# Kernel tuning notes

Hardware: AMD Instinct MI355X
Metric: run time of the kernel (lower is better)

The kernel has to match this reference:

```python
import jax, jax.numpy as jnp
import numpy as np

N_NODES = 100000

def gcn_conv(x, W, b, src, dst, n_nodes):
    # PyG GCNConv: out[dst] += norm * (x @ W)[src] + b, with self-loops and
    # symmetric normalization norm = deg^-1/2[src] * deg^-1/2[dst].
    loop = jnp.arange(n_nodes, dtype=src.dtype)
    s = jnp.concatenate([src, loop])
    d = jnp.concatenate([dst, loop])
    deg = jax.ops.segment_sum(jnp.ones_like(d, dtype=x.dtype), d, num_segments=n_nodes)
    dinv = jnp.where(deg > 0, jax.lax.rsqrt(deg), 0.0)
    norm = dinv[s] * dinv[d]                      # [E+N]
    h = x @ W                                     # [N, H]
    msg = h[s] * norm[:, None]                    # [E+N, H] gather
    out = jax.ops.segment_sum(msg, d, num_segments=n_nodes)  # scatter-add
    return out + b

def setup_inputs() -> dict:
    key = jax.random.key(0)
    ks = jax.random.split(key, 8)
    in_dim, hidden = 128, 128
    x = jax.random.normal(ks[0], (N_NODES, in_dim), dtype=jnp.float32)
    edge_index = jax.random.randint(ks[1], (2, 1600000), 0, N_NODES, dtype=jnp.int32)
    sc = 1.0 / np.sqrt(in_dim)
    W1 = jax.random.uniform(ks[2], (in_dim, hidden), jnp.float32, -sc, sc)
    b1 = jnp.zeros((hidden,), jnp.float32)
    W2 = jax.random.uniform(ks[3], (hidden, hidden), jnp.float32, -sc, sc)
    b2 = jnp.zeros((hidden,), jnp.float32)
    Wf = jax.random.uniform(ks[4], (hidden, 1), jnp.float32, -sc, sc)
    bf = jnp.zeros((1,), jnp.float32)
    return {"x": x, "W1": W1, "b1": b1, "W2": W2, "b2": b2, "Wf": Wf, "bf": bf, "edge_index": edge_index}

def reference(x, W1, b1, W2, b2, Wf, bf, edge_index):
    src, dst = edge_index[0], edge_index[1]
    h = jax.nn.relu(gcn_conv(x, W1, b1, src, dst, N_NODES))
    h = jax.nn.relu(gcn_conv(h, W2, b2, src, dst, N_NODES))
    out = (h @ Wf + bf).squeeze(-1)               # [N]
    return out
```

## Files before the change

### kernel.cpp

```cpp
#include <hip/hip_runtime.h>


#define FEAT 128
#define BSH 9
#define BNODES 512

typedef __attribute__((ext_vector_type(8))) short  bf16x8;
typedef __attribute__((ext_vector_type(4))) float  f32x4;

static inline size_t align_up(size_t x, size_t a){ return (x + a - 1) & ~(a - 1); }

__device__ __forceinline__ unsigned short f2bf(float f){
  unsigned int u = __float_as_uint(f);
  return (unsigned short)((u + 0x7fffu + ((u >> 16) & 1u)) >> 16);
}
__device__ __forceinline__ float bflo(unsigned int p){ return __uint_as_float(p << 16); }
__device__ __forceinline__ float bfhi(unsigned int p){ return __uint_as_float(p & 0xffff0000u); }


__global__ __launch_bounds__(256) void bin_count_kernel(
    const int* __restrict__ dst, int* __restrict__ bucket_cnt, int E, int chunk)
{
  __shared__ int hist[256];
  int t = threadIdx.x;
  hist[t] = 0;
  __syncthreads();
  int s0 = blockIdx.x * chunk, s1 = min(E, s0 + chunk);
  for (int i = s0 + t; i < s1; i += 256) atomicAdd(&hist[dst[i] >> BSH], 1);
  __syncthreads();
  if (hist[t] > 0) atomicAdd(&bucket_cnt[t], hist[t]);
}

__global__ __launch_bounds__(256) void bucket_scan_kernel(
    int* __restrict__ bucket_cnt, int* __restrict__ bucket_off,
    int* __restrict__ bucket_cur, int* __restrict__ rowptr, int nbk, int N)
{
  __shared__ int sh[256];
  int t = threadIdx.x;
  int v = (t < nbk) ? bucket_cnt[t] : 0;
  sh[t] = v;
  __syncthreads();
  #pragma unroll
  for (int off = 1; off < 256; off <<= 1){
    int add = (t >= off) ? sh[t - off] : 0;
    __syncthreads();
    sh[t] += add;
    __syncthreads();
  }
  if (t < nbk){
    int e = sh[t] - v;
    bucket_off[t] = e;
    bucket_cur[t] = e;
  }
  if (t == 0){
    bucket_off[nbk] = sh[255];
    rowptr[N] = sh[255];
  }
}

__global__ __launch_bounds__(256) void bin_scatter_kernel(
    const int* __restrict__ src, const int* __restrict__ dst,
    int* __restrict__ bucket_cur, unsigned int* __restrict__ packed, int E, int chunk)
{
  __shared__ int hist[256];
  __shared__ int base[256];
  int t = threadIdx.x;
  hist[t] = 0;
  __syncthreads();
  int s0 = blockIdx.x * chunk, s1 = min(E, s0 + chunk);
  for (int i = s0 + t; i < s1; i += 256) atomicAdd(&hist[dst[i] >> BSH], 1);
  __syncthreads();
  int h = hist[t];
  if (h > 0) base[t] = atomicAdd(&bucket_cur[t], h);
  __syncthreads();
  hist[t] = 0;
  __syncthreads();
  for (int i = s0 + t; i < s1; i += 256){
    int d = dst[i];
    int b = d >> BSH;
    int pos = base[b] + atomicAdd(&hist[b], 1);
    packed[pos] = ((unsigned int)src[i] << BSH) | (unsigned int)(d & (BNODES - 1));
  }
}

__global__ __launch_bounds__(512) void bucket_build_kernel(
    const unsigned int* __restrict__ packed, const int* __restrict__ bucket_off,
    float* __restrict__ dinv, int* __restrict__ rowptr, int* __restrict__ colidx, int N)
{
  __shared__ int degl[BNODES];
  __shared__ int scan[BNODES];
  __shared__ int cur[BNODES];
  int b = blockIdx.x;
  int t = threadIdx.x;
  int node0 = b << BSH;
  int e0 = bucket_off[b], e1 = bucket_off[b + 1];

  degl[t] = 0;
  __syncthreads();
  for (int i = e0 + t; i < e1; i += BNODES) atomicAdd(&degl[packed[i] & (BNODES - 1)], 1);
  __syncthreads();

  int d = degl[t];
  int node = node0 + t;
  if (node < N) dinv[node] = rsqrtf((float)(d + 1));

  scan[t] = d;
  __syncthreads();
  #pragma unroll
  for (int off = 1; off < BNODES; off <<= 1){
    int add = (t >= off) ? scan[t - off] : 0;
    __syncthreads();
    scan[t] += add;
    __syncthreads();
  }
  int excl = scan[t] - d;
  if (node < N) rowptr[node] = e0 + excl;
  cur[t] = excl;
  __syncthreads();

  for (int i = e0 + t; i < e1; i += BNODES){
    unsigned int p = packed[i];
    int pos = atomicAdd(&cur[p & (BNODES - 1)], 1);
    colidx[e0 + pos] = (int)(p >> BSH);
  }
}


__global__ __launch_bounds__(256) void wt_convert_kernel(
    const float* __restrict__ W, unsigned short* __restrict__ Wt)
{
  int gid = blockIdx.x * 256 + threadIdx.x;
  int n = gid >> 7, k = gid & 127;
  Wt[gid] = f2bf(W[(size_t)k * FEAT + n]);
}


template<bool INBF>
__global__ __launch_bounds__(256) void gemm_mfma_kernel(
    const void* __restrict__ Ain, const unsigned short* __restrict__ Wt,
    const float* __restrict__ dinv, unsigned short* __restrict__ Cout, int N)
{
  __shared__ unsigned short aT[128 * 128];
  __shared__ unsigned short wT[128 * 128];
  const int t = threadIdx.x;
  const int row0 = blockIdx.x * 128;

  {
    const uint4* s4 = (const uint4*)Wt;
    #pragma unroll
    for (int i = 0; i < 8; ++i){
      int c = t + i * 256;
      int n = c >> 4, k8 = (c & 15) * 8;
      uint4 v = s4[c];
      *reinterpret_cast<uint4*>(&wT[(n * 128 + k8) ^ ((n & 7) << 3)]) = v;
    }
  }
  if (INBF){
    const unsigned short* Ab = (const unsigned short*)Ain;
    #pragma unroll
    for (int i = 0; i < 8; ++i){
      int c = t + i * 256;
      int r = c >> 4, k8 = (c & 15) * 8;
      int row = row0 + r;
      uint4 v = make_uint4(0, 0, 0, 0);
      float s = 0.f;
      if (row < N){ v = *(const uint4*)(Ab + (size_t)row * FEAT + k8); s = dinv[row]; }
      unsigned int wi[4] = {v.x, v.y, v.z, v.w}, o[4];
      #pragma unroll
      for (int j = 0; j < 4; ++j){
        float lo = bflo(wi[j]) * s, hi = bfhi(wi[j]) * s;
        o[j] = (unsigned int)f2bf(lo) | ((unsigned int)f2bf(hi) << 16);
      }
      *reinterpret_cast<uint4*>(&aT[(r * 128 + k8) ^ ((r & 7) << 3)]) = make_uint4(o[0], o[1], o[2], o[3]);
    }
  } else {
    const float* Af = (const float*)Ain;
    #pragma unroll
    for (int i = 0; i < 16; ++i){
      int c = t + i * 256;
      int r = c >> 5, k4 = (c & 31) * 4;
      int row = row0 + r;
      float4 v = make_float4(0, 0, 0, 0);
      float s = 0.f;
      if (row < N){ v = *(const float4*)(Af + (size_t)row * FEAT + k4); s = dinv[row]; }
      ushort4 o;
      o.x = f2bf(v.x * s); o.y = f2bf(v.y * s); o.z = f2bf(v.z * s); o.w = f2bf(v.w * s);
      *reinterpret_cast<ushort4*>(&aT[(r * 128 + k4) ^ ((r & 7) << 3)]) = o;
    }
  }
  __syncthreads();

  const int w = t >> 6, l = t & 63;
  const int wbase = w * 32;
  const int lm = l & 15;
  const int lk = (l >> 4) * 8;

  f32x4 acc[8][2];
  #pragma unroll
  for (int mt = 0; mt < 8; ++mt)
    #pragma unroll
    for (int nt = 0; nt < 2; ++nt) acc[mt][nt] = (f32x4){0.f, 0.f, 0.f, 0.f};

  #pragma unroll
  for (int ks = 0; ks < 4; ++ks){
    int kb = ks * 32 + lk;
    bf16x8 bfr[2], afr[8];
    #pragma unroll
    for (int nt = 0; nt < 2; ++nt){
      int n = wbase + nt * 16 + lm;
      bfr[nt] = *reinterpret_cast<const bf16x8*>(&wT[(n * 128 + kb) ^ ((n & 7) << 3)]);
    }
    #pragma unroll
    for (int mt = 0; mt < 8; ++mt){
      int m = mt * 16 + lm;
      afr[mt] = *reinterpret_cast<const bf16x8*>(&aT[(m * 128 + kb) ^ ((m & 7) << 3)]);
    }
    #pragma unroll
    for (int mt = 0; mt < 8; ++mt)
      #pragma unroll
      for (int nt = 0; nt < 2; ++nt)
        acc[mt][nt] = __builtin_amdgcn_mfma_f32_16x16x32_bf16(afr[mt], bfr[nt], acc[mt][nt], 0, 0, 0);
  }
  __syncthreads();

  #pragma unroll
  for (int mt = 0; mt < 8; ++mt)
    #pragma unroll
    for (int nt = 0; nt < 2; ++nt)
      #pragma unroll
      for (int r = 0; r < 4; ++r){
        int mrow = mt * 16 + (l >> 4) * 4 + r;
        int col  = wbase + nt * 16 + lm;
        aT[mrow * 128 + col] = f2bf(acc[mt][nt][r]);
      }
  __syncthreads();
  #pragma unroll
  for (int i = 0; i < 8; ++i){
    int c = t + i * 256;
    int r = c >> 4, k8 = (c & 15) * 8;
    int row = row0 + r;
    if (row < N)
      *reinterpret_cast<uint4*>(&Cout[(size_t)row * FEAT + k8]) =
          *reinterpret_cast<const uint4*>(&aT[r * 128 + k8]);
  }
}


__global__ __launch_bounds__(256) void aggregate_kernel(
    const unsigned short* __restrict__ Hs, const int* __restrict__ rowptr,
    const int* __restrict__ col, const float* __restrict__ dinv,
    const float* __restrict__ bias, unsigned short* __restrict__ out, int N)
{
  int gid  = blockIdx.x * blockDim.x + threadIdx.x;
  int v    = gid >> 6;
  int lane = threadIdx.x & 63;
  if (v >= N) return;
  const float dv = dinv[v];
  const unsigned int* Hu = (const unsigned int*)Hs;
  int e = rowptr[v], end = rowptr[v + 1];

  unsigned int m = Hu[(size_t)v * 64 + lane];
  float ax = bflo(m), ay = bfhi(m);
  for (; e + 4 <= end; e += 4){
    int u0 = col[e], u1 = col[e + 1], u2 = col[e + 2], u3 = col[e + 3];
    unsigned int p0 = Hu[(size_t)u0 * 64 + lane];
    unsigned int p1 = Hu[(size_t)u1 * 64 + lane];
    unsigned int p2 = Hu[(size_t)u2 * 64 + lane];
    unsigned int p3 = Hu[(size_t)u3 * 64 + lane];
    ax += bflo(p0) + bflo(p1) + bflo(p2) + bflo(p3);
    ay += bfhi(p0) + bfhi(p1) + bfhi(p2) + bfhi(p3);
  }
  for (; e < end; ++e){
    unsigned int p = Hu[(size_t)col[e] * 64 + lane];
    ax += bflo(p); ay += bfhi(p);
  }
  float2 b = *reinterpret_cast<const float2*>(bias + lane * 2);
  float ox = fmaxf(dv * ax + b.x, 0.f);
  float oy = fmaxf(dv * ay + b.y, 0.f);
  ((unsigned int*)out)[(size_t)v * 64 + lane] =
      (unsigned int)f2bf(ox) | ((unsigned int)f2bf(oy) << 16);
}

__global__ __launch_bounds__(256) void aggregate_final_kernel(
    const unsigned short* __restrict__ Hs, const int* __restrict__ rowptr,
    const int* __restrict__ col, const float* __restrict__ dinv,
    const float* __restrict__ bias, const float* __restrict__ Wf,
    const float* __restrict__ bf, float* __restrict__ out, int N)
{
  int gid  = blockIdx.x * blockDim.x + threadIdx.x;
  int v    = gid >> 6;
  int lane = threadIdx.x & 63;
  if (v >= N) return;
  const float dv = dinv[v];
  const unsigned int* Hu = (const unsigned int*)Hs;
  int e = rowptr[v], end = rowptr[v + 1];

  unsigned int m = Hu[(size_t)v * 64 + lane];
  float ax = bflo(m), ay = bfhi(m);
  for (; e + 4 <= end; e += 4){
    int u0 = col[e], u1 = col[e + 1], u2 = col[e + 2], u3 = col[e + 3];
    unsigned int p0 = Hu[(size_t)u0 * 64 + lane];
    unsigned int p1 = Hu[(size_t)u1 * 64 + lane];
    unsigned int p2 = Hu[(size_t)u2 * 64 + lane];
    unsigned int p3 = Hu[(size_t)u3 * 64 + lane];
    ax += bflo(p0) + bflo(p1) + bflo(p2) + bflo(p3);
    ay += bfhi(p0) + bfhi(p1) + bfhi(p2) + bfhi(p3);
  }
  for (; e < end; ++e){
    unsigned int p = Hu[(size_t)col[e] * 64 + lane];
    ax += bflo(p); ay += bfhi(p);
  }
  float2 b = *reinterpret_cast<const float2*>(bias + lane * 2);
  float ox = fmaxf(dv * ax + b.x, 0.f);
  float oy = fmaxf(dv * ay + b.y, 0.f);
  float2 wf = *reinterpret_cast<const float2*>(Wf + lane * 2);
  float p = ox * wf.x + oy * wf.y;
  #pragma unroll
  for (int off = 32; off > 0; off >>= 1) p += __shfl_down(p, off, 64);
  if (lane == 0) out[v] = p + bf[0];
}


extern "C" void kernel_launch(void* const* d_in, const int* in_sizes, int n_in,
                              void* d_out, int out_size, void* d_ws, size_t ws_size,
                              hipStream_t stream)
{
  const float* x   = (const float*)d_in[0];
  const float* W1  = (const float*)d_in[1];
  const float* b1  = (const float*)d_in[2];
  const float* W2  = (const float*)d_in[3];
  const float* b2  = (const float*)d_in[4];
  const float* Wf  = (const float*)d_in[5];
  const float* bfb = (const float*)d_in[6];
  const int*  eidx = (const int*)d_in[7];

  const int N = in_sizes[0] / FEAT;
  const int E = in_sizes[7] / 2;
  const int* src = eidx;
  const int* dst = eidx + E;
  const int NBK = (N + BNODES - 1) >> BSH;

  char* ws = (char*)d_ws;
  size_t off = 0;
  auto alloc = [&](size_t bytes){ void* p = ws + off; off = align_up(off + bytes, 256); return p; };
  unsigned short* A    = (unsigned short*)alloc((size_t)N * FEAT * 2);
  unsigned short* B    = (unsigned short*)alloc((size_t)N * FEAT * 2);
  unsigned short* Wt1  = (unsigned short*)alloc((size_t)FEAT * FEAT * 2);
  unsigned short* Wt2  = (unsigned short*)alloc((size_t)FEAT * FEAT * 2);
  float* dinv   = (float*)alloc((size_t)N * 4);
  int*   rowptr = (int*)  alloc((size_t)(N + 1) * 4);
  int*   colidx = (int*)  alloc((size_t)E * 4);
  unsigned int* packed = (unsigned int*)alloc((size_t)E * 4);
  int*   bcnt   = (int*)  alloc(256 * 4);
  int*   boff   = (int*)  alloc(257 * 4);
  int*   bcur   = (int*)  alloc(256 * 4);
  (void)ws_size; (void)n_in; (void)out_size;

  const int tb = 256;
  const int PBLK = 256;
  const int chunk = (E + PBLK - 1) / PBLK;

  hipMemsetAsync(bcnt, 0, 256 * 4, stream);

  bin_count_kernel  <<<PBLK, 256, 0, stream>>>(dst, bcnt, E, chunk);
  bucket_scan_kernel<<<1, 256, 0, stream>>>(bcnt, boff, bcur, rowptr, NBK, N);
  bin_scatter_kernel<<<PBLK, 256, 0, stream>>>(src, dst, bcur, packed, E, chunk);
  bucket_build_kernel<<<NBK, BNODES, 0, stream>>>(packed, boff, dinv, rowptr, colidx, N);

  wt_convert_kernel<<<64, 256, 0, stream>>>(W1, Wt1);
  wt_convert_kernel<<<64, 256, 0, stream>>>(W2, Wt2);

  int gblocks = (N + 127) / 128;
  int ablocks = (int)(((size_t)N * 64 + tb - 1) / tb);

  gemm_mfma_kernel<false><<<gblocks, 256, 0, stream>>>(x, Wt1, dinv, A, N);
  aggregate_kernel<<<ablocks, tb, 0, stream>>>(A, rowptr, colidx, dinv, b1, B, N);
  gemm_mfma_kernel<true><<<gblocks, 256, 0, stream>>>(B, Wt2, dinv, A, N);
  aggregate_final_kernel<<<ablocks, tb, 0, stream>>>(A, rowptr, colidx, dinv, b2, Wf, bfb,
                                                     (float*)d_out, N);
}
```

Before: 344.3 us.

## Split each node's edges across two half-wavefronts with 8-byte gathers

Each 64-lane wavefront now covers one node as two 32-lane halves. Each half takes alternate edges and loads 8 bytes (4 bf16 features) per lane, and the halves combine with a cross-half shuffle. The inner loop is unrolled to 8 outstanding gathers per half, so more independent row fetches are in flight to hide gather latency. In exchange it adds a shuffle reduction and idles half the lanes in the epilogue.

```diff
diff --git a/kernel.cpp b/kernel.cpp
--- a/kernel.cpp
+++ b/kernel.cpp
@@ -246,6 +246,45 @@
 }
 
 
+#define AGG_BODY(Hq, vrow)                                                    \
+  float a0 = 0.f, a1 = 0.f, a2 = 0.f, a3 = 0.f;                               \
+  if (half == 0){                                                             \
+    uint2 s = Hq[(size_t)(vrow) * 32 + hl];                                   \
+    a0 = bflo(s.x); a1 = bfhi(s.x); a2 = bflo(s.y); a3 = bfhi(s.y);           \
+  }                                                                           \
+  int i = e0 + half;                                                          \
+  for (; i + 14 < end; i += 16){                                              \
+    int u0=col[i],u1=col[i+2],u2=col[i+4],u3=col[i+6];                        \
+    int u4=col[i+8],u5=col[i+10],u6=col[i+12],u7=col[i+14];                   \
+    uint2 p0=Hq[(size_t)u0*32+hl], p1=Hq[(size_t)u1*32+hl];                   \
+    uint2 p2=Hq[(size_t)u2*32+hl], p3=Hq[(size_t)u3*32+hl];                   \
+    uint2 p4=Hq[(size_t)u4*32+hl], p5=Hq[(size_t)u5*32+hl];                   \
+    uint2 p6=Hq[(size_t)u6*32+hl], p7=Hq[(size_t)u7*32+hl];                   \
+    a0 += bflo(p0.x)+bflo(p1.x)+bflo(p2.x)+bflo(p3.x)                         \
+        + bflo(p4.x)+bflo(p5.x)+bflo(p6.x)+bflo(p7.x);                        \
+    a1 += bfhi(p0.x)+bfhi(p1.x)+bfhi(p2.x)+bfhi(p3.x)                         \
+        + bfhi(p4.x)+bfhi(p5.x)+bfhi(p6.x)+bfhi(p7.x);                        \
+    a2 += bflo(p0.y)+bflo(p1.y)+bflo(p2.y)+bflo(p3.y)                         \
+        + bflo(p4.y)+bflo(p5.y)+bflo(p6.y)+bflo(p7.y);                        \
+    a3 += bfhi(p0.y)+bfhi(p1.y)+bfhi(p2.y)+bfhi(p3.y)                         \
+        + bfhi(p4.y)+bfhi(p5.y)+bfhi(p6.y)+bfhi(p7.y);                        \
+  }                                                                           \
+  for (; i + 6 < end; i += 8){                                                \
+    int u0=col[i],u1=col[i+2],u2=col[i+4],u3=col[i+6];                        \
+    uint2 p0=Hq[(size_t)u0*32+hl], p1=Hq[(size_t)u1*32+hl];                   \
+    uint2 p2=Hq[(size_t)u2*32+hl], p3=Hq[(size_t)u3*32+hl];                   \
+    a0 += bflo(p0.x)+bflo(p1.x)+bflo(p2.x)+bflo(p3.x);                        \
+    a1 += bfhi(p0.x)+bfhi(p1.x)+bfhi(p2.x)+bfhi(p3.x);                        \
+    a2 += bflo(p0.y)+bflo(p1.y)+bflo(p2.y)+bflo(p3.y);                        \
+    a3 += bfhi(p0.y)+bfhi(p1.y)+bfhi(p2.y)+bfhi(p3.y);                        \
+  }                                                                           \
+  for (; i < end; i += 2){                                                    \
+    uint2 p = Hq[(size_t)col[i]*32 + hl];                                     \
+    a0 += bflo(p.x); a1 += bfhi(p.x); a2 += bflo(p.y); a3 += bfhi(p.y);       \
+  }                                                                           \
+  a0 += __shfl_xor(a0, 32, 64); a1 += __shfl_xor(a1, 32, 64);                 \
+  a2 += __shfl_xor(a2, 32, 64); a3 += __shfl_xor(a3, 32, 64);
+
 __global__ __launch_bounds__(256) void aggregate_kernel(
     const unsigned short* __restrict__ Hs, const int* __restrict__ rowptr,
     const int* __restrict__ col, const float* __restrict__ dinv,
@@ -253,32 +292,27 @@
 {
   int gid  = blockIdx.x * blockDim.x + threadIdx.x;
   int v    = gid >> 6;
+  if (v >= N) return;
   int lane = threadIdx.x & 63;
-  if (v >= N) return;
-  const float dv = dinv[v];
-  const unsigned int* Hu = (const unsigned int*)Hs;
-  int e = rowptr[v], end = rowptr[v + 1];
-
-  unsigned int m = Hu[(size_t)v * 64 + lane];
-  float ax = bflo(m), ay = bfhi(m);
-  for (; e + 4 <= end; e += 4){
-    int u0 = col[e], u1 = col[e + 1], u2 = col[e + 2], u3 = col[e + 3];
-    unsigned int p0 = Hu[(size_t)u0 * 64 + lane];
-    unsigned int p1 = Hu[(size_t)u1 * 64 + lane];
-    unsigned int p2 = Hu[(size_t)u2 * 64 + lane];
-    unsigned int p3 = Hu[(size_t)u3 * 64 + lane];
-    ax += bflo(p0) + bflo(p1) + bflo(p2) + bflo(p3);
-    ay += bfhi(p0) + bfhi(p1) + bfhi(p2) + bfhi(p3);
-  }
-  for (; e < end; ++e){
-    unsigned int p = Hu[(size_t)col[e] * 64 + lane];
-    ax += bflo(p); ay += bfhi(p);
-  }
-  float2 b = *reinterpret_cast<const float2*>(bias + lane * 2);
-  float ox = fmaxf(dv * ax + b.x, 0.f);
-  float oy = fmaxf(dv * ay + b.y, 0.f);
-  ((unsigned int*)out)[(size_t)v * 64 + lane] =
-      (unsigned int)f2bf(ox) | ((unsigned int)f2bf(oy) << 16);
+  int half = lane >> 5;
+  int hl   = lane & 31;
+  const uint2* Hq = (const uint2*)Hs;
+  int e0 = rowptr[v], end = rowptr[v + 1];
+
+  AGG_BODY(Hq, v)
+
+  if (half == 0){
+    float dv = dinv[v];
+    float4 b = reinterpret_cast<const float4*>(bias)[hl];
+    float o0 = fmaxf(dv * a0 + b.x, 0.f);
+    float o1 = fmaxf(dv * a1 + b.y, 0.f);
+    float o2 = fmaxf(dv * a2 + b.z, 0.f);
+    float o3 = fmaxf(dv * a3 + b.w, 0.f);
+    uint2 o;
+    o.x = (unsigned int)f2bf(o0) | ((unsigned int)f2bf(o1) << 16);
+    o.y = (unsigned int)f2bf(o2) | ((unsigned int)f2bf(o3) << 16);
+    reinterpret_cast<uint2*>(out)[(size_t)v * 32 + hl] = o;
+  }
 }
 
 __global__ __launch_bounds__(256) void aggregate_final_kernel(
@@ -289,35 +323,28 @@
 {
   int gid  = blockIdx.x * blockDim.x + threadIdx.x;
   int v    = gid >> 6;
+  if (v >= N) return;
   int lane = threadIdx.x & 63;
-  if (v >= N) return;
-  const float dv = dinv[v];
-  const unsigned int* Hu = (const unsigned int*)Hs;
-  int e = rowptr[v], end = rowptr[v + 1];
-
-  unsigned int m = Hu[(size_t)v * 64 + lane];
-  float ax = bflo(m), ay = bfhi(m);
-  for (; e + 4 <= end; e += 4){
-    int u0 = col[e], u1 = col[e + 1], u2 = col[e + 2], u3 = col[e + 3];
-    unsigned int p0 = Hu[(size_t)u0 * 64 + lane];
-    unsigned int p1 = Hu[(size_t)u1 * 64 + lane];
-    unsigned int p2 = Hu[(size_t)u2 * 64 + lane];
-    unsigned int p3 = Hu[(size_t)u3 * 64 + lane];
-    ax += bflo(p0) + bflo(p1) + bflo(p2) + bflo(p3);
-    ay += bfhi(p0) + bfhi(p1) + bfhi(p2) + bfhi(p3);
-  }
-  for (; e < end; ++e){
-    unsigned int p = Hu[(size_t)col[e] * 64 + lane];
-    ax += bflo(p); ay += bfhi(p);
-  }
-  float2 b = *reinterpret_cast<const float2*>(bias + lane * 2);
-  float ox = fmaxf(dv * ax + b.x, 0.f);
-  float oy = fmaxf(dv * ay + b.y, 0.f);
-  float2 wf = *reinterpret_cast<const float2*>(Wf + lane * 2);
-  float p = ox * wf.x + oy * wf.y;
-  #pragma unroll
-  for (int off = 32; off > 0; off >>= 1) p += __shfl_down(p, off, 64);
-  if (lane == 0) out[v] = p + bf[0];
+  int half = lane >> 5;
+  int hl   = lane & 31;
+  const uint2* Hq = (const uint2*)Hs;
+  int e0 = rowptr[v], end = rowptr[v + 1];
+
+  AGG_BODY(Hq, v)
+
+  if (half == 0){
+    float dv = dinv[v];
+    float4 b  = reinterpret_cast<const float4*>(bias)[hl];
+    float4 wf = reinterpret_cast<const float4*>(Wf)[hl];
+    float o0 = fmaxf(dv * a0 + b.x, 0.f);
+    float o1 = fmaxf(dv * a1 + b.y, 0.f);
+    float o2 = fmaxf(dv * a2 + b.z, 0.f);
+    float o3 = fmaxf(dv * a3 + b.w, 0.f);
+    float p = o0 * wf.x + o1 * wf.y + o2 * wf.z + o3 * wf.w;
+    #pragma unroll
+    for (int off = 16; off > 0; off >>= 1) p += __shfl_down(p, off, 32);
+    if (hl == 0) out[v] = p + bf[0];
+  }
 }
 
 
```

Measured after the change: 323.8 us. 1.06x faster.
